# Optimization experiments

Hardware: AMD Instinct MI355X
Metric: run time of the kernel (lower is better)

## Reference

```python
import jax, jax.numpy as jnp
import numpy as np

EMBED_DIM = 768
NUM_HEAD = 12
HEAD_DIM = EMBED_DIM // NUM_HEAD


def setup_inputs() -> dict:
    key = jax.random.key(0)
    ks = jax.random.split(key, 9)
    B, S, E = 1, 4096, EMBED_DIM
    s = 1.0 / np.sqrt(E)
    inp = {
        "x": jax.random.normal(ks[0], (B, S, E), dtype=jnp.float32),
        "mask": jnp.zeros((B, S), dtype=jnp.bool_),  # True = masked out (padding)
        "Wq": jax.random.normal(ks[1], (E, E), dtype=jnp.float32) * s,
        "bq": jnp.zeros((E,), dtype=jnp.float32),
        "Wk": jax.random.normal(ks[2], (E, E), dtype=jnp.float32) * s,
        "bk": jnp.zeros((E,), dtype=jnp.float32),
        "Wv": jax.random.normal(ks[3], (E, E), dtype=jnp.float32) * s,
        "bv": jnp.zeros((E,), dtype=jnp.float32),
        "Wo": jax.random.normal(ks[4], (E, E), dtype=jnp.float32) * s,
        "bo": jnp.zeros((E,), dtype=jnp.float32),
    }
    return inp


def reference(x, mask, Wq, bq, Wk, bk, Wv, bv, Wo, bo):
    B, S, E = x.shape
    H, D = NUM_HEAD, HEAD_DIM
    # QKV projections -> [B, H, S, D]
    q = (x @ Wq.T + bq).reshape(B, S, H, D).transpose(0, 2, 1, 3)
    k = (x @ Wk.T + bk).reshape(B, S, H, D).transpose(0, 2, 1, 3)
    v = (x @ Wv.T + bv).reshape(B, S, H, D).transpose(0, 2, 1, 3)
    # NOTE: original scales by sqrt(embed_dim), not sqrt(head_dim)
    attn = jnp.einsum("bhqd,bhkd->bhqk", q, k) / jnp.sqrt(jnp.float32(E))
    # mask: [B, S] -> broadcast over (head, query) dims; True -> -inf
    attn = jnp.where(mask[:, None, None, :], -jnp.inf, attn)
    attn = jax.nn.softmax(attn, axis=-1)  # same math as manual max-subtract softmax
    out = jnp.einsum("bhqk,bhkd->bhqd", attn, v)  # [B, H, S, D]
    out = out.transpose(0, 2, 1, 3).reshape(B, S, E)
    return out @ Wo.T + bo
```

## Files before the change

kernel.cpp:

```cpp
#include <hip/hip_runtime.h>
#include <hip/hip_bf16.h>
#include <math.h>

typedef __bf16 bf16;
typedef __attribute__((ext_vector_type(8))) __bf16 bf16x8;
typedef __attribute__((ext_vector_type(4))) __bf16 bf16x4;
typedef __attribute__((ext_vector_type(4))) float f32x4;
typedef __attribute__((ext_vector_type(16))) float f32x16;

typedef __attribute__((address_space(1))) void* as1ptr;
typedef __attribute__((address_space(3))) void* as3ptr;

__device__ __forceinline__ void gload16(const void* g, void* lds) {
  __builtin_amdgcn_global_load_lds((as1ptr)(unsigned long long)(g),
                                   (as3ptr)(unsigned long long)(lds), 16, 0, 0);
}

#define MFMA16(a, b, c) __builtin_amdgcn_mfma_f32_16x16x32_bf16((a), (b), (c), 0, 0, 0)
#define MFMA32(a, b, c) __builtin_amdgcn_mfma_f32_32x32x16_bf16((a), (b), (c), 0, 0, 0)
#define EXP2(x) __builtin_amdgcn_exp2f(x)
#define WAITV4 asm volatile("s_waitcnt vmcnt(4)" ::: "memory")
#define WAITV0 asm volatile("s_waitcnt vmcnt(0)" ::: "memory")
#define BAR() __builtin_amdgcn_s_barrier()
#define PRIO1() __builtin_amdgcn_s_setprio(1)
#define PRIO0() __builtin_amdgcn_s_setprio(0)

#define SEQ 4096
#define EMB 768
#define QSC (0.036084391824351615f * 1.4426950408889634f)

#define NCVT 2688
__global__ __launch_bounds__(256)
void cvt_all_kernel(const float* __restrict__ x, const float* __restrict__ Wq,
                    const float* __restrict__ Wk, const float* __restrict__ Wv,
                    const float* __restrict__ Wo,
                    bf16* __restrict__ xb, bf16* __restrict__ Wqb, bf16* __restrict__ Wkb,
                    bf16* __restrict__ Wvb, bf16* __restrict__ Wob,
                    const unsigned char* __restrict__ mask,
                    unsigned long long* __restrict__ tf64) {
  int b = blockIdx.x;
  if (b == NCVT) {
    int t = threadIdx.x;
    if (t < 64) {
      unsigned v = 0;
      const unsigned char* mp = mask + t * 64;
      for (int i = 0; i < 64; i++) v |= mp[i];
      unsigned long long bits = __ballot(v != 0);
      if (t == 0) *tf64 = bits;
    }
    return;
  }
  const float* in;
  bf16* out;
  int base;
  if (b < 1536) {
    in = x; out = xb; base = b;
  } else {
    int r = b - 1536, seg = r / 288, off = r % 288;
    in  = (seg == 0) ? Wq  : (seg == 1) ? Wk  : (seg == 2) ? Wv  : Wo;
    out = (seg == 0) ? Wqb : (seg == 1) ? Wkb : (seg == 2) ? Wvb : Wob;
    base = off;
  }
  int i = (base * 256 + threadIdx.x) * 8;
  float4 a = *(const float4*)(in + i);
  float4 c = *(const float4*)(in + i + 4);
  bf16x8 v;
  v[0] = (bf16)a.x; v[1] = (bf16)a.y; v[2] = (bf16)a.z; v[3] = (bf16)a.w;
  v[4] = (bf16)c.x; v[5] = (bf16)c.y; v[6] = (bf16)c.z; v[7] = (bf16)c.w;
  *(bf16x8*)(out + i) = v;
}

template <int MODE>
__global__ __launch_bounds__(256)
void gemm_bt_kernel(const bf16* __restrict__ A,
                    const bf16* __restrict__ B0, const bf16* __restrict__ B1,
                    const bf16* __restrict__ B2,
                    const float* __restrict__ bias0, const float* __restrict__ bias1,
                    const float* __restrict__ bias2,
                    float* __restrict__ outF, bf16* __restrict__ Qh,
                    char* __restrict__ Kswz, char* __restrict__ Vswz) {
  __shared__ __attribute__((aligned(16))) char Asb[3][8192];
  __shared__ __attribute__((aligned(16))) char Bsb[3][8192];
  const int tid = threadIdx.x;
  const int wid = tid >> 6, lane = tid & 63;
  const int g = lane >> 4, c16 = lane & 15;
  const int wr = wid >> 1, wc = wid & 1;
  const int bm0 = blockIdx.x * 128;

  const bf16* Bp;
  const float* bias;
  int nb, mat = 0;
  if (MODE == 1) {
    mat = blockIdx.y / 6;
    nb = (blockIdx.y % 6) * 128;
    Bp = (mat == 0) ? B0 : (mat == 1 ? B1 : B2);
    bias = (mat == 0) ? bias0 : (mat == 1 ? bias1 : bias2);
  } else {
    nb = blockIdx.y * 128;
    Bp = B0;
    bias = bias0;
  }

  const int arow = tid >> 2, acol = (tid & 3) * 16;

#define STAGE_G(k, b)                                                              \
  do {                                                                             \
    gload16((const char*)A + (size_t)(bm0 + arow) * (EMB * 2) + (k)*64 + acol,     \
            &Asb[b][wid * 1024]);                                                  \
    gload16((const char*)A + (size_t)(bm0 + 64 + arow) * (EMB * 2) + (k)*64 + acol,\
            &Asb[b][4096 + wid * 1024]);                                           \
    gload16((const char*)Bp + (size_t)(nb + arow) * (EMB * 2) + (k)*64 + acol,     \
            &Bsb[b][wid * 1024]);                                                  \
    gload16((const char*)Bp + (size_t)(nb + 64 + arow) * (EMB * 2) + (k)*64 + acol,\
            &Bsb[b][4096 + wid * 1024]);                                           \
  } while (0)

  f32x4 acc[4][4];
#pragma unroll
  for (int i = 0; i < 4; i++)
#pragma unroll
    for (int j = 0; j < 4; j++) acc[i][j] = f32x4{0.f, 0.f, 0.f, 0.f};

#define COMPUTE_G(cur)                                                         \
  do {                                                                         \
    bf16x8 a[4], b[4];                                                         \
    _Pragma("unroll") for (int i = 0; i < 4; i++)                              \
        a[i] = *(const bf16x8*)(&Asb[cur][(wr * 64 + i * 16 + c16) * 64 + g * 16]); \
    _Pragma("unroll") for (int j = 0; j < 4; j++)                              \
        b[j] = *(const bf16x8*)(&Bsb[cur][(wc * 64 + j * 16 + c16) * 64 + g * 16]); \
    PRIO1();                                                                   \
    _Pragma("unroll") for (int i = 0; i < 4; i++)                              \
        _Pragma("unroll") for (int j = 0; j < 4; j++)                          \
            acc[i][j] = MFMA16(a[i], b[j], acc[i][j]);                         \
    PRIO0();                                                                   \
  } while (0)

  STAGE_G(0, 0);
  STAGE_G(1, 1);
  int cur = 0;
  for (int kk = 0; kk < EMB / 32 - 1; ++kk) {
    WAITV4;
    BAR();
    if (kk < EMB / 32 - 2) {
      int stb = (cur == 0) ? 2 : cur - 1;
      STAGE_G(kk + 2, stb);
    }
    COMPUTE_G(cur);
    cur = (cur == 2) ? 0 : cur + 1;
  }
  WAITV0;
  BAR();
  COMPUTE_G(cur);
#undef STAGE_G
#undef COMPUTE_G

#pragma unroll
  for (int i = 0; i < 4; i++) {
#pragma unroll
    for (int j = 0; j < 4; j++) {
      int colL = nb + wc * 64 + j * 16 + c16;
      float bval = bias[colL];
#pragma unroll
      for (int r = 0; r < 4; r++) {
        int row = bm0 + wr * 64 + i * 16 + 4 * g + r;
        float val = acc[i][j][r] + bval;
        if (MODE == 0) {
          outF[(size_t)row * EMB + colL] = val;
        } else {
          int hh = colL >> 6, d = colL & 63;
          if (mat == 0) {
            Qh[((size_t)hh * SEQ + row) * 64 + d] = (bf16)(val * QSC);
          } else if (mat == 1) {
            *(bf16*)(Kswz + ((size_t)hh * SEQ + row) * 128 +
                     ((d * 2) ^ ((row & 7) << 4))) = (bf16)val;
          } else {
            int kk2 = row & 63;
            int cc = (kk2 & 48) | (kk2 & 3) | ((kk2 & 4) << 1) | ((kk2 & 8) >> 1);
            *(bf16*)(Vswz + ((size_t)hh * 64 + d) * 8192 + (size_t)(row >> 6) * 128 +
                     ((cc * 2) ^ ((d & 7) << 4))) = (bf16)val;
          }
        }
      }
    }
  }
}

__global__ __launch_bounds__(256)
void attn_kernel(const char* __restrict__ Kswz, const char* __restrict__ Vswz,
                 const bf16* __restrict__ Qh, const unsigned char* __restrict__ mask,
                 const unsigned long long* __restrict__ tf64, bf16* __restrict__ O) {
  __shared__ __attribute__((aligned(16))) char Kt[3][8192];
  __shared__ __attribute__((aligned(16))) char Vt[3][8192];
  const int tid = threadIdx.x;
  const int wid = tid >> 6, lane = tid & 63;
  const int qh = wid >> 1, kh = wid & 1;
  const int l31 = lane & 31, hi = lane >> 5;
  const int bsw = (blockIdx.x & 7) * 96 + (blockIdx.x >> 3);
  const int h = bsw >> 6;
  const int q0 = (bsw & 63) * 64;
  const unsigned long long tfb = *tf64;

  bf16x8 qa[4];
  {
    const bf16* qp = Qh + ((size_t)h * SEQ + q0 + qh * 32 + l31) * 64 + hi * 8;
    qa[0] = *(const bf16x8*)(qp);
    qa[1] = *(const bf16x8*)(qp + 16);
    qa[2] = *(const bf16x8*)(qp + 32);
    qa[3] = *(const bf16x8*)(qp + 48);
  }

  f32x16 ot0, ot1;
#pragma unroll
  for (int r = 0; r < 16; r++) { ot0[r] = 0.f; ot1[r] = 0.f; }
  float m_ = -1e38f, l_ = 0.f;

  const char* ksrc = Kswz + (size_t)h * SEQ * 128 + tid * 16;
  const char* vsrc0 = Vswz + ((size_t)h * 64 + (tid >> 3)) * 8192 + (tid & 7) * 16;
  const char* vsrc1 = Vswz + ((size_t)h * 64 + 32 + (tid >> 3)) * 8192 + (tid & 7) * 16;

#define STAGE(t, b)                                                    \
  do {                                                                 \
    gload16(ksrc + (size_t)(t)*8192,        &Kt[b][wid * 1024]);       \
    gload16(ksrc + (size_t)(t)*8192 + 4096, &Kt[b][4096 + wid * 1024]);\
    gload16(vsrc0 + (size_t)(t)*128, &Vt[b][wid * 1024]);              \
    gload16(vsrc1 + (size_t)(t)*128, &Vt[b][4096 + wid * 1024]);       \
  } while (0)

  const int krow = kh * 32 + l31;
  const int ksw = (krow & 7) << 4;
  const int vsw = (l31 & 7) << 4;
  const int vcb = kh * 64 + hi * 16;

#define COMPUTE(t, cur)                                                          \
  do {                                                                           \
    const char* Kb = Kt[cur];                                                    \
    const char* Vb = Vt[cur];                                                    \
    bf16x8 kf0 = *(const bf16x8*)(Kb + krow * 128 + ((hi * 16) ^ ksw));          \
    bf16x8 kf1 = *(const bf16x8*)(Kb + krow * 128 + ((32 + hi * 16) ^ ksw));     \
    bf16x8 kf2 = *(const bf16x8*)(Kb + krow * 128 + ((64 + hi * 16) ^ ksw));     \
    bf16x8 kf3 = *(const bf16x8*)(Kb + krow * 128 + ((96 + hi * 16) ^ ksw));     \
    f32x16 s;                                                                    \
    _Pragma("unroll") for (int r = 0; r < 16; r++) s[r] = 0.f;                   \
    PRIO1();                                                                     \
    s = MFMA32(kf0, qa[0], s);                                                   \
    s = MFMA32(kf1, qa[1], s);                                                   \
    s = MFMA32(kf2, qa[2], s);                                                   \
    s = MFMA32(kf3, qa[3], s);                                                   \
    PRIO0();                                                                     \
    if (tfb & (1ull << (t))) {                                                   \
      _Pragma("unroll") for (int r = 0; r < 16; r++) {                           \
        int key = (t)*64 + kh * 32 + (r & 3) + 8 * (r >> 2) + 4 * hi;            \
        if (mask[key]) s[r] = -INFINITY;                                         \
      }                                                                          \
    }                                                                            \
    float m01 = fmaxf(fmaxf(s[0], s[1]), fmaxf(s[2], s[3]));                     \
    float m23 = fmaxf(fmaxf(s[4], s[5]), fmaxf(s[6], s[7]));                     \
    float m45 = fmaxf(fmaxf(s[8], s[9]), fmaxf(s[10], s[11]));                   \
    float m67 = fmaxf(fmaxf(s[12], s[13]), fmaxf(s[14], s[15]));                 \
    float mt = fmaxf(fmaxf(m01, m23), fmaxf(m45, m67));                          \
    mt = fmaxf(mt, __shfl_xor(mt, 32));                                          \
    if (__any(mt > m_ + 8.f)) {                                                  \
      float mn = fmaxf(m_, mt);                                                  \
      float corr = EXP2(m_ - mn);                                                \
      l_ *= corr;                                                                \
      ot0 *= corr;                                                               \
      ot1 *= corr;                                                               \
      m_ = mn;                                                                   \
    }                                                                            \
    float p[16];                                                                 \
    _Pragma("unroll") for (int r = 0; r < 16; r++) p[r] = EXP2(s[r] - m_);       \
    float ls = (((p[0] + p[1]) + (p[2] + p[3])) + ((p[4] + p[5]) + (p[6] + p[7]))) + \
               (((p[8] + p[9]) + (p[10] + p[11])) + ((p[12] + p[13]) + (p[14] + p[15]))); \
    ls += __shfl_xor(ls, 32);                                                    \
    l_ += ls;                                                                    \
    bf16x8 pb0, pb1;                                                             \
    _Pragma("unroll") for (int e = 0; e < 8; ++e) {                              \
      pb0[e] = (bf16)p[e];                                                       \
      pb1[e] = (bf16)p[8 + e];                                                   \
    }                                                                            \
    bf16x8 vf00 = *(const bf16x8*)(Vb + l31 * 128 + ((vcb) ^ vsw));              \
    bf16x8 vf01 = *(const bf16x8*)(Vb + l31 * 128 + ((vcb + 32) ^ vsw));         \
    bf16x8 vf10 = *(const bf16x8*)(Vb + (32 + l31) * 128 + ((vcb) ^ vsw));       \
    bf16x8 vf11 = *(const bf16x8*)(Vb + (32 + l31) * 128 + ((vcb + 32) ^ vsw));  \
    PRIO1();                                                                     \
    ot0 = MFMA32(vf00, pb0, ot0);                                                \
    ot0 = MFMA32(vf01, pb1, ot0);                                                \
    ot1 = MFMA32(vf10, pb0, ot1);                                                \
    ot1 = MFMA32(vf11, pb1, ot1);                                                \
    PRIO0();                                                                     \
  } while (0)

  STAGE(0, 0);
  STAGE(1, 1);
  int cur = 0;
  for (int t = 0; t < SEQ / 64 - 1; ++t) {
    WAITV4;
    BAR();
    if (t < SEQ / 64 - 2) {
      int stb = (cur == 0) ? 2 : cur - 1;
      STAGE(t + 2, stb);
    }
    COMPUTE(t, cur);
    cur = (cur == 2) ? 0 : cur + 1;
  }
  WAITV0;
  BAR();
  COMPUTE(SEQ / 64 - 1, cur);
#undef STAGE
#undef COMPUTE

  __syncthreads();
  float* ml = (float*)&Vt[0][0];
  ml[(wid * 64 + lane) * 2 + 0] = m_;
  ml[(wid * 64 + lane) * 2 + 1] = l_;
  __syncthreads();
  const int pw = wid ^ 1;
  float m2 = ml[(pw * 64 + lane) * 2 + 0];
  float l2 = ml[(pw * 64 + lane) * 2 + 1];
  float M = fmaxf(m_, m2);
  float al = EXP2(m_ - M);
  float lt = al * l_ + EXP2(m2 - M) * l2;
  ot0 *= al;
  ot1 *= al;
  char* ob = (char*)&Kt[0][0];
  char* obase = ob + qh * 8192 + lane * 128;
  const int osw = (lane & 7) << 4;
  if (kh == 1) {
#pragma unroll
    for (int u = 0; u < 4; ++u) {
      f32x4 w0 = {ot0[4 * u], ot0[4 * u + 1], ot0[4 * u + 2], ot0[4 * u + 3]};
      f32x4 w1 = {ot1[4 * u], ot1[4 * u + 1], ot1[4 * u + 2], ot1[4 * u + 3]};
      *(f32x4*)(obase + ((u * 16) ^ osw)) = w0;
      *(f32x4*)(obase + (((4 + u) * 16) ^ osw)) = w1;
    }
  }
  __syncthreads();
  if (kh == 0) {
    float inv = 1.f / lt;
    int tok = q0 + qh * 32 + l31;
    bf16* op = O + (size_t)tok * EMB + h * 64;
#pragma unroll
    for (int u = 0; u < 4; ++u) {
      f32x4 w0 = *(const f32x4*)(obase + ((u * 16) ^ osw));
      f32x4 w1 = *(const f32x4*)(obase + (((4 + u) * 16) ^ osw));
      bf16x4 o0, o1;
#pragma unroll
      for (int e = 0; e < 4; ++e) {
        o0[e] = (bf16)((ot0[4 * u + e] + w0[e]) * inv);
        o1[e] = (bf16)((ot1[4 * u + e] + w1[e]) * inv);
      }
      *(bf16x4*)(op + 8 * u + 4 * hi) = o0;
      *(bf16x4*)(op + 32 + 8 * u + 4 * hi) = o1;
    }
  }
}

extern "C" void kernel_launch(void* const* d_in, const int* in_sizes, int n_in,
                              void* d_out, int out_size, void* d_ws, size_t ws_size,
                              hipStream_t stream) {
  (void)in_sizes; (void)n_in; (void)out_size; (void)ws_size;
  const float* x = (const float*)d_in[0];
  const unsigned char* mask = (const unsigned char*)d_in[1];
  const float* Wq = (const float*)d_in[2];
  const float* bq = (const float*)d_in[3];
  const float* Wk = (const float*)d_in[4];
  const float* bk = (const float*)d_in[5];
  const float* Wv = (const float*)d_in[6];
  const float* bv = (const float*)d_in[7];
  const float* Wo = (const float*)d_in[8];
  const float* bo = (const float*)d_in[9];
  float* out = (float*)d_out;
  char* ws = (char*)d_ws;

  bf16* xb   = (bf16*)(ws + 0);
  bf16* Wqb  = (bf16*)(ws + 6291456);
  bf16* Wkb  = (bf16*)(ws + 7471104);
  bf16* Wvb  = (bf16*)(ws + 8650752);
  bf16* Wob  = (bf16*)(ws + 9830400);
  bf16* Qh   = (bf16*)(ws + 11010048);
  char* Kswz = ws + 17301504;
  char* Vswz = ws + 23592960;
  bf16* Obuf = (bf16*)(ws + 29884416);
  unsigned long long* tf64 = (unsigned long long*)(ws + 36175872);

  cvt_all_kernel<<<NCVT + 1, 256, 0, stream>>>(x, Wq, Wk, Wv, Wo, xb, Wqb, Wkb, Wvb,
                                               Wob, mask, tf64);
  gemm_bt_kernel<1><<<dim3(32, 18), 256, 0, stream>>>(
      xb, Wqb, Wkb, Wvb, bq, bk, bv, nullptr, Qh, Kswz, Vswz);
  attn_kernel<<<768, 256, 0, stream>>>(Kswz, Vswz, Qh, mask, tf64, Obuf);
  gemm_bt_kernel<0><<<dim3(32, 6), 256, 0, stream>>>(
      Obuf, Wob, nullptr, nullptr, bo, nullptr, nullptr, out, nullptr, nullptr, nullptr);
}
```

Baseline: 142.4 us.

## Split attention over two key halves with 128-query blocks and merge kernel

The attention kernel now runs 512-thread blocks covering 128 queries, and each block handles only half of the key sequence (split-K), so every block's serial loop is half as long. Each K/V tile is staged with one load per thread and shared by twice as many query waves, which cuts global K/V traffic per query. Each split writes a normalized partial output plus its row max and sum. A new merge kernel combines the two partials with softmax rescaling. The cost is an extra launch, partial-output writes and reads (reusing the x buffer), and more LDS and waves per block.

```diff
diff --git a/kernel.cpp b/kernel.cpp
--- a/kernel.cpp
+++ b/kernel.cpp
@@ -20,6 +20,7 @@
 #define MFMA32(a, b, c) __builtin_amdgcn_mfma_f32_32x32x16_bf16((a), (b), (c), 0, 0, 0)
 #define EXP2(x) __builtin_amdgcn_exp2f(x)
 #define WAITV4 asm volatile("s_waitcnt vmcnt(4)" ::: "memory")
+#define WAITV2 asm volatile("s_waitcnt vmcnt(2)" ::: "memory")
 #define WAITV0 asm volatile("s_waitcnt vmcnt(0)" ::: "memory")
 #define BAR() __builtin_amdgcn_s_barrier()
 #define PRIO1() __builtin_amdgcn_s_setprio(1)
@@ -185,24 +186,29 @@
   }
 }
 
-__global__ __launch_bounds__(256)
+__global__ __launch_bounds__(512)
 void attn_kernel(const char* __restrict__ Kswz, const char* __restrict__ Vswz,
                  const bf16* __restrict__ Qh, const unsigned char* __restrict__ mask,
-                 const unsigned long long* __restrict__ tf64, bf16* __restrict__ O) {
-  __shared__ __attribute__((aligned(16))) char Kt[3][8192];
-  __shared__ __attribute__((aligned(16))) char Vt[3][8192];
+                 const unsigned long long* __restrict__ tf64,
+                 bf16* __restrict__ P0, bf16* __restrict__ P1, float* __restrict__ lm) {
+  __shared__ __attribute__((aligned(16))) char LBUF[49152];
+  char* LK = LBUF;
+  char* LV = LBUF + 24576;
   const int tid = threadIdx.x;
   const int wid = tid >> 6, lane = tid & 63;
   const int qh = wid >> 1, kh = wid & 1;
   const int l31 = lane & 31, hi = lane >> 5;
-  const int bsw = (blockIdx.x & 7) * 96 + (blockIdx.x >> 3);
+  const int bsw = ((blockIdx.x & 7) * 96) + (blockIdx.x >> 3);
   const int h = bsw >> 6;
-  const int q0 = (bsw & 63) * 64;
+  const int rem = bsw & 63;
+  const int qb = rem >> 1;
+  const int ks = rem & 1;
   const unsigned long long tfb = *tf64;
+  const int NT = 32;
 
   bf16x8 qa[4];
   {
-    const bf16* qp = Qh + ((size_t)h * SEQ + q0 + qh * 32 + l31) * 64 + hi * 8;
+    const bf16* qp = Qh + ((size_t)h * SEQ + qb * 128 + qh * 32 + l31) * 64 + hi * 8;
     qa[0] = *(const bf16x8*)(qp);
     qa[1] = *(const bf16x8*)(qp + 16);
     qa[2] = *(const bf16x8*)(qp + 32);
@@ -214,16 +220,13 @@
   for (int r = 0; r < 16; r++) { ot0[r] = 0.f; ot1[r] = 0.f; }
   float m_ = -1e38f, l_ = 0.f;
 
-  const char* ksrc = Kswz + (size_t)h * SEQ * 128 + tid * 16;
-  const char* vsrc0 = Vswz + ((size_t)h * 64 + (tid >> 3)) * 8192 + (tid & 7) * 16;
-  const char* vsrc1 = Vswz + ((size_t)h * 64 + 32 + (tid >> 3)) * 8192 + (tid & 7) * 16;
-
-#define STAGE(t, b)                                                    \
-  do {                                                                 \
-    gload16(ksrc + (size_t)(t)*8192,        &Kt[b][wid * 1024]);       \
-    gload16(ksrc + (size_t)(t)*8192 + 4096, &Kt[b][4096 + wid * 1024]);\
-    gload16(vsrc0 + (size_t)(t)*128, &Vt[b][wid * 1024]);              \
-    gload16(vsrc1 + (size_t)(t)*128, &Vt[b][4096 + wid * 1024]);       \
+  const char* ksrc = Kswz + (size_t)h * SEQ * 128 + (size_t)ks * 2048 * 128 + tid * 16;
+  const char* vsrc = Vswz + ((size_t)h * 64 + (tid >> 3)) * 8192 + ks * 4096 + (tid & 7) * 16;
+
+#define STAGE(t, b)                                              \
+  do {                                                           \
+    gload16(ksrc + (size_t)(t)*8192, LK + (b)*8192 + wid * 1024);\
+    gload16(vsrc + (size_t)(t)*128,  LV + (b)*8192 + wid * 1024);\
   } while (0)
 
   const int krow = kh * 32 + l31;
@@ -233,8 +236,8 @@
 
 #define COMPUTE(t, cur)                                                          \
   do {                                                                           \
-    const char* Kb = Kt[cur];                                                    \
-    const char* Vb = Vt[cur];                                                    \
+    const char* Kb = LK + (cur)*8192;                                            \
+    const char* Vb = LV + (cur)*8192;                                            \
     bf16x8 kf0 = *(const bf16x8*)(Kb + krow * 128 + ((hi * 16) ^ ksw));          \
     bf16x8 kf1 = *(const bf16x8*)(Kb + krow * 128 + ((32 + hi * 16) ^ ksw));     \
     bf16x8 kf2 = *(const bf16x8*)(Kb + krow * 128 + ((64 + hi * 16) ^ ksw));     \
@@ -247,9 +250,9 @@
     s = MFMA32(kf2, qa[2], s);                                                   \
     s = MFMA32(kf3, qa[3], s);                                                   \
     PRIO0();                                                                     \
-    if (tfb & (1ull << (t))) {                                                   \
+    if (tfb & (1ull << (ks * 32 + (t)))) {                                       \
       _Pragma("unroll") for (int r = 0; r < 16; r++) {                           \
-        int key = (t)*64 + kh * 32 + (r & 3) + 8 * (r >> 2) + 4 * hi;            \
+        int key = ks * 2048 + (t)*64 + kh * 32 + (r & 3) + 8 * (r >> 2) + 4 * hi;\
         if (mask[key]) s[r] = -INFINITY;                                         \
       }                                                                          \
     }                                                                            \
@@ -293,10 +296,10 @@
   STAGE(0, 0);
   STAGE(1, 1);
   int cur = 0;
-  for (int t = 0; t < SEQ / 64 - 1; ++t) {
-    WAITV4;
+  for (int t = 0; t < NT - 1; ++t) {
+    WAITV2;
     BAR();
-    if (t < SEQ / 64 - 2) {
+    if (t < NT - 2) {
       int stb = (cur == 0) ? 2 : cur - 1;
       STAGE(t + 2, stb);
     }
@@ -305,12 +308,12 @@
   }
   WAITV0;
   BAR();
-  COMPUTE(SEQ / 64 - 1, cur);
+  COMPUTE(NT - 1, cur);
 #undef STAGE
 #undef COMPUTE
 
   __syncthreads();
-  float* ml = (float*)&Vt[0][0];
+  float* ml = (float*)(LBUF + 32768);
   ml[(wid * 64 + lane) * 2 + 0] = m_;
   ml[(wid * 64 + lane) * 2 + 1] = l_;
   __syncthreads();
@@ -322,8 +325,7 @@
   float lt = al * l_ + EXP2(m2 - M) * l2;
   ot0 *= al;
   ot1 *= al;
-  char* ob = (char*)&Kt[0][0];
-  char* obase = ob + qh * 8192 + lane * 128;
+  char* obase = LBUF + qh * 8192 + lane * 128;
   const int osw = (lane & 7) << 4;
   if (kh == 1) {
 #pragma unroll
@@ -337,8 +339,9 @@
   __syncthreads();
   if (kh == 0) {
     float inv = 1.f / lt;
-    int tok = q0 + qh * 32 + l31;
-    bf16* op = O + (size_t)tok * EMB + h * 64;
+    int tok = qb * 128 + qh * 32 + l31;
+    bf16* Op = ks ? P1 : P0;
+    bf16* op = Op + (size_t)tok * EMB + h * 64;
 #pragma unroll
     for (int u = 0; u < 4; ++u) {
       f32x4 w0 = *(const f32x4*)(obase + ((u * 16) ^ osw));
@@ -352,7 +355,37 @@
       *(bf16x4*)(op + 8 * u + 4 * hi) = o0;
       *(bf16x4*)(op + 32 + 8 * u + 4 * hi) = o1;
     }
-  }
+    if (lane < 32) {
+      float* lmp = lm + (((size_t)ks * 12 + h) * 4096 + tok) * 2;
+      lmp[0] = M;
+      lmp[1] = lt;
+    }
+  }
+}
+
+__global__ __launch_bounds__(256)
+void merge_kernel(bf16* __restrict__ P0, const bf16* __restrict__ P1,
+                  const float* __restrict__ lm) {
+  int idx = (blockIdx.x * 256 + threadIdx.x) * 8;
+  int tok = idx / EMB;
+  int e0 = idx % EMB;
+  int h = e0 >> 6;
+  const float* l0p = lm + ((size_t)h * 4096 + tok) * 2;
+  const float* l1p = lm + (((size_t)12 + h) * 4096 + tok) * 2;
+  float m0 = l0p[0], l0 = l0p[1];
+  float m1 = l1p[0], l1 = l1p[1];
+  float M = fmaxf(m0, m1);
+  float w0 = EXP2(m0 - M) * l0;
+  float w1 = EXP2(m1 - M) * l1;
+  float inv = 1.f / (w0 + w1);
+  w0 *= inv;
+  w1 *= inv;
+  bf16x8 a = *(const bf16x8*)(P0 + idx);
+  bf16x8 b = *(const bf16x8*)(P1 + idx);
+  bf16x8 o;
+#pragma unroll
+  for (int e = 0; e < 8; ++e) o[e] = (bf16)(w0 * (float)a[e] + w1 * (float)b[e]);
+  *(bf16x8*)(P0 + idx) = o;
 }
 
 extern "C" void kernel_launch(void* const* d_in, const int* in_sizes, int n_in,
@@ -382,12 +415,15 @@
   char* Vswz = ws + 23592960;
   bf16* Obuf = (bf16*)(ws + 29884416);
   unsigned long long* tf64 = (unsigned long long*)(ws + 36175872);
+  float* lmArr = (float*)(ws + 36179968);
+  bf16* P1 = xb;
 
   cvt_all_kernel<<<NCVT + 1, 256, 0, stream>>>(x, Wq, Wk, Wv, Wo, xb, Wqb, Wkb, Wvb,
                                                Wob, mask, tf64);
   gemm_bt_kernel<1><<<dim3(32, 18), 256, 0, stream>>>(
       xb, Wqb, Wkb, Wvb, bq, bk, bv, nullptr, Qh, Kswz, Vswz);
-  attn_kernel<<<768, 256, 0, stream>>>(Kswz, Vswz, Qh, mask, tf64, Obuf);
+  attn_kernel<<<768, 512, 0, stream>>>(Kswz, Vswz, Qh, mask, tf64, Obuf, P1, lmArr);
+  merge_kernel<<<1536, 256, 0, stream>>>(Obuf, P1, lmArr);
   gemm_bt_kernel<0><<<dim3(32, 6), 256, 0, stream>>>(
       Obuf, Wob, nullptr, nullptr, bo, nullptr, nullptr, out, nullptr, nullptr, nullptr);
 }
```

After: 134.2 us. -5.8%, faster.
